# Optimization experiments

Measured on AMD Instinct MI355X. Metric: run time of the kernel, lower is better.

The kernel has to match this reference:

```python
import jax, jax.numpy as jnp
import numpy as np

B, F, T, D, W = 65536, 8, 60, 10, 6  # batch, features, time, window, n_windows
EPS = 1e-8
BN_EPS = 1e-5
IU, JU = np.triu_indices(F, k=1)  # 28 feature pairs


def _bn1d(x, g, b):
    # training-mode BatchNorm1d over [B, C, L]: stats over (B, L) per channel
    m = x.mean(axis=(0, 2), keepdims=True)
    v = x.var(axis=(0, 2), keepdims=True)
    return (x - m) * jax.lax.rsqrt(v + BN_EPS) * g[None, :, None] + b[None, :, None]


def setup_inputs() -> dict:
    key = jax.random.key(0)
    ks = jax.random.split(key, 8)
    s = 0.1
    return {
        "xb": jax.random.normal(ks[0], (B, 1, F, T), dtype=jnp.float32),
        "conv_w": jax.random.normal(ks[1], (4, 1, 1, D), dtype=jnp.float32) * s,
        "conv_b": jnp.zeros((4,), jnp.float32),
        "bn1_g": jnp.ones((28,), jnp.float32), "bn1_b": jnp.zeros((28,), jnp.float32),
        "bn4_g": jnp.ones((F,), jnp.float32), "bn4_b": jnp.zeros((F,), jnp.float32),
        "bn6_g": jnp.ones((F,), jnp.float32), "bn6_b": jnp.zeros((F,), jnp.float32),
        "bn9_g": jnp.ones((32,), jnp.float32), "bn9_b": jnp.zeros((32,), jnp.float32),
        "bnmax_g": jnp.ones((76,), jnp.float32), "bnmax_b": jnp.zeros((76,), jnp.float32),
        "w1": jax.random.normal(ks[2], (30, 608), dtype=jnp.float32) * s,
        "b1": jnp.zeros((30,), jnp.float32),
        "w2": jax.random.normal(ks[3], (1, 30), dtype=jnp.float32) * s,
        "b2": jnp.zeros((1,), jnp.float32),
    }


def reference(xb, conv_w, conv_b, bn1_g, bn1_b, bn4_g, bn4_b, bn6_g, bn6_b,
              bn9_g, bn9_b, bnmax_g, bnmax_b, w1, b1, w2, b2):
    b = xb.shape[0]
    xw = xb.reshape(b, F, W, D)  # non-overlapping windows of length D=10

    # ts_corr: pairwise Pearson correlation per window -> [b, 28, W]
    mu = xw.mean(axis=-1, keepdims=True)
    c = xw - mu
    cov = jnp.einsum('bfwt,bgwt->bfgw', c, c) / D          # [b,F,F,W]
    std = jnp.sqrt((c * c).mean(axis=-1) + EPS)            # [b,F,W]
    corr = cov / (std[:, :, None, :] * std[:, None, :, :] + EPS)
    xb1 = corr[:, IU, JU, :]                               # [b,28,W]

    # ts_zscore: mean/std per window -> [b, F, W]
    xb4 = mu[..., 0] / (std + EPS)

    # ts_decaylinear: linear-decay weighted mean -> [b, F, W]
    dw = jnp.arange(1, D + 1, dtype=jnp.float32)
    dw = dw / dw.sum()
    xb6 = jnp.einsum('bfwt,t->bfw', xw, dw)

    # conv2d kernel (1,10) stride (1,10) -> [b, 4*F, W]
    xb9 = jnp.einsum('bfwt,ot->bofw', xw, conv_w[:, 0, 0, :]) + conv_b[None, :, None, None]
    xb9 = xb9.reshape(b, 4 * F, W)

    h = jnp.concatenate([
        _bn1d(xb1, bn1_g, bn1_b),
        _bn1d(xb4, bn4_g, bn4_b),
        _bn1d(xb6, bn6_g, bn6_b),
        _bn1d(xb9, bn9_g, bn9_b),
    ], axis=1)                                             # [b,76,6]

    h_max = h.reshape(b, 76, 2, 3).max(axis=-1)            # MaxPool1d(3,3) -> [b,76,2]
    h_max = _bn1d(h_max, bnmax_g, bnmax_b)

    flat = jnp.concatenate([h.reshape(b, -1), h_max.reshape(b, -1)], axis=1)  # [b,608]
    out = jax.nn.relu(flat @ w1.T + b1) @ w2.T + b2
    return out.reshape(-1)
```

## Files before the change

kernel.cpp:

```cpp
#include <hip/hip_runtime.h>


#define EPS_F    1e-8f
#define BN_EPS_F 1e-5f
#define LSTR 82

__device__ __forceinline__ float frcp(float x) {
  return __builtin_amdgcn_rcpf(x);
}

template<int Ctrl, int RowMask>
__device__ __forceinline__ float dpp_mov0(float v) {
  return __int_as_float(__builtin_amdgcn_update_dpp(
      0, __float_as_int(v), Ctrl, RowMask, 0xf, true));
}
__device__ __forceinline__ float wave_sum64(float v) {
  v += dpp_mov0<0x111, 0xf>(v);
  v += dpp_mov0<0x112, 0xf>(v);
  v += dpp_mov0<0x114, 0xf>(v);
  v += dpp_mov0<0x118, 0xf>(v);
  v += dpp_mov0<0x142, 0xa>(v);
  v += dpp_mov0<0x143, 0xc>(v);
  return v;
}

constexpr int PI_[28] = {0,0,0,0,0,0,0, 1,1,1,1,1,1, 2,2,2,2,2, 3,3,3,3, 4,4,4, 5,5, 6};
constexpr int PJ_[28] = {1,2,3,4,5,6,7, 2,3,4,5,6,7, 3,4,5,6,7, 4,5,6,7, 5,6,7, 6,7, 7};

template<int PASS, int W>
__device__ __forceinline__ void corr_step(
    const float* __restrict__ bx, const int w,
    const float* __restrict__ w1s,
    float* __restrict__ S, float* __restrict__ Q, float* __restrict__ M,
    float* __restrict__ A, float* __restrict__ partial,
    const int bid, const int lane)
{
  constexpr int PLO = W * 14;
  constexpr int FLO = W * 4;
  float sum[8], SD[8], SP[14];
  #pragma unroll
  for (int f = 0; f < 8; ++f) { sum[f] = 0.f; SD[f] = 0.f; }
  #pragma unroll
  for (int k = 0; k < 14; ++k) SP[k] = 0.f;
  #pragma unroll
  for (int tp = 0; tp < 5; ++tp) {
    float2 x2[8];
    #pragma unroll
    for (int f = 0; f < 8; ++f)
      x2[f] = *reinterpret_cast<const float2*>(bx + f*10 + tp*2);
    #pragma unroll
    for (int f = 0; f < 8; ++f) {
      sum[f] += x2[f].x + x2[f].y;
      SD[f] = fmaf(x2[f].x, x2[f].x, fmaf(x2[f].y, x2[f].y, SD[f]));
    }
    #pragma unroll
    for (int k = 0; k < 14; ++k) {
      const int i = PI_[PLO + k], j = PJ_[PLO + k];
      SP[k] = fmaf(x2[i].x, x2[j].x, fmaf(x2[i].y, x2[j].y, SP[k]));
    }
  }
  float mu[8], sd[8];
  #pragma unroll
  for (int f = 0; f < 8; ++f) {
    mu[f] = sum[f] * 0.1f;
    sd[f] = sqrtf(fmaf(-mu[f], mu[f], SD[f] * 0.1f) + EPS_F);
  }
  #pragma unroll
  for (int k = 0; k < 14; ++k) {
    const int i = PI_[PLO + k], j = PJ_[PLO + k];
    float cov = fmaf(-mu[i], mu[j], SP[k] * 0.1f);
    float v = cov * frcp(fmaf(sd[i], sd[j], EPS_F));
    M[k] = fmaxf(M[k], v);
    if (PASS == 0) { S[k] += v; Q[k] = fmaf(v, v, Q[k]); }
    else {
      const float* wr = w1s + ((PLO + k)*6 + w) * 30;
      #pragma unroll
      for (int j2 = 0; j2 < 30; ++j2) A[j2] = fmaf(v, wr[j2], A[j2]);
    }
  }
  #pragma unroll
  for (int q = 0; q < 4; ++q) {
    const int k = 14 + q;
    float v = mu[FLO + q] * frcp(sd[FLO + q] + EPS_F);
    M[k] = fmaxf(M[k], v);
    if (PASS == 0) { S[k] += v; Q[k] = fmaf(v, v, Q[k]); }
    else {
      const float* wr = w1s + ((28 + FLO + q)*6 + w) * 30;
      #pragma unroll
      for (int j2 = 0; j2 < 30; ++j2) A[j2] = fmaf(v, wr[j2], A[j2]);
    }
  }
  if (w == 2 || w == 5) {
    const int h = (w == 5);
    #pragma unroll
    for (int k = 0; k < 18; ++k) {
      const int ch = (k < 14) ? (PLO + k) : (28 + FLO + (k - 14));
      if (PASS == 0) {
        float t2 = wave_sum64(M[k]);
        float t3 = wave_sum64(M[k] * M[k]);
        if (lane == 63) {
          partial[(size_t)(152 + ch) * 2048 + h*1024 + bid] = t2;
          partial[(size_t)(228 + ch) * 2048 + h*1024 + bid] = t3;
        }
      } else {
        const float* wr = w1s + (456 + ch*2 + h) * 30;
        #pragma unroll
        for (int j2 = 0; j2 < 30; ++j2) A[j2] = fmaf(M[k], wr[j2], A[j2]);
      }
      M[k] = -3.0e38f;
    }
  }
}

template<int PASS>
__device__ __forceinline__ void bc_step(
    const float* __restrict__ bx, const int w, const int G,
    const float* __restrict__ cw, const float* __restrict__ cb,
    const float* __restrict__ w1s,
    float* __restrict__ S, float* __restrict__ Q, float* __restrict__ M,
    float* __restrict__ A, float* __restrict__ partial,
    const int bid, const int lane)
{
  const int FLO = G * 4;
  #pragma unroll
  for (int q = 0; q < 4; ++q) {
    const int f = FLO + q;
    float2 x2[5];
    #pragma unroll
    for (int tp = 0; tp < 5; ++tp)
      x2[tp] = *reinterpret_cast<const float2*>(bx + f*10 + tp*2);
    float wsm = 0.f;
    #pragma unroll
    for (int tp = 0; tp < 5; ++tp)
      wsm = fmaf(x2[tp].x, (float)(2*tp+1) * (1.f/55.f),
            fmaf(x2[tp].y, (float)(2*tp+2) * (1.f/55.f), wsm));
    {
      const int k = q*5;
      M[k] = fmaxf(M[k], wsm);
      if (PASS == 0) { S[k] += wsm; Q[k] = fmaf(wsm, wsm, Q[k]); }
      else {
        const float* wr = w1s + ((36 + f)*6 + w) * 30;
        #pragma unroll
        for (int j2 = 0; j2 < 30; ++j2) A[j2] = fmaf(wsm, wr[j2], A[j2]);
      }
    }
    #pragma unroll
    for (int o = 0; o < 4; ++o) {
      float cv = cb[o];
      #pragma unroll
      for (int tp = 0; tp < 5; ++tp)
        cv = fmaf(x2[tp].x, cw[o*10 + 2*tp], fmaf(x2[tp].y, cw[o*10 + 2*tp + 1], cv));
      const int k = q*5 + 1 + o;
      M[k] = fmaxf(M[k], cv);
      if (PASS == 0) { S[k] += cv; Q[k] = fmaf(cv, cv, Q[k]); }
      else {
        const float* wr = w1s + ((44 + o*8 + f)*6 + w) * 30;
        #pragma unroll
        for (int j2 = 0; j2 < 30; ++j2) A[j2] = fmaf(cv, wr[j2], A[j2]);
      }
    }
  }
  if (w == 2 || w == 5) {
    const int h = (w == 5);
    #pragma unroll
    for (int k = 0; k < 20; ++k) {
      const int f = FLO + k/5, c = k%5;
      const int ch = (c == 0) ? (36 + f) : (44 + (c-1)*8 + f);
      if (PASS == 0) {
        float t2 = wave_sum64(M[k]);
        float t3 = wave_sum64(M[k] * M[k]);
        if (lane == 63) {
          partial[(size_t)(152 + ch) * 2048 + h*1024 + bid] = t2;
          partial[(size_t)(228 + ch) * 2048 + h*1024 + bid] = t3;
        }
      } else {
        const float* wr = w1s + (456 + ch*2 + h) * 30;
        #pragma unroll
        for (int j2 = 0; j2 < 30; ++j2) A[j2] = fmaf(M[k], wr[j2], A[j2]);
      }
      M[k] = -3.0e38f;
    }
  }
}


template<int PASS>
__global__ void __launch_bounds__(256, 2)
apass(const float* __restrict__ xb, const float* __restrict__ cw,
      const float* __restrict__ cb, const float* __restrict__ w1s,
      const float* __restrict__ c0, const float* __restrict__ w2,
      const float* __restrict__ b2, float* __restrict__ partial,
      float* __restrict__ out)
{
  __shared__ float sx[64 * LSTR];
  const int tid  = threadIdx.x;
  const int wave = __builtin_amdgcn_readfirstlane(tid >> 6);
  const int lane = tid & 63;
  const int bid  = blockIdx.x;

  float A[30], S[20], Q[20], M[20];
  if (PASS == 0) {
    #pragma unroll
    for (int k = 0; k < 20; ++k) { S[k] = 0.f; Q[k] = 0.f; }
  } else {
    #pragma unroll
    for (int j = 0; j < 30; ++j) A[j] = 0.f;
  }
  #pragma unroll
  for (int k = 0; k < 20; ++k) M[k] = -3.0e38f;

  const int sq = tid >> 2, qq = tid & 3;
  const float* gbase = xb + (size_t)bid * (64*480) + sq*480 + qq*120;
  float* lbase = sx + sq*LSTR + qq*20;
  const float* bx = sx + lane * LSTR;

  #pragma unroll 1
  for (int w = 0; w < 6; ++w) {
    float2 t[10];
    #pragma unroll
    for (int k = 0; k < 10; ++k)
      t[k] = *reinterpret_cast<const float2*>(gbase + w*10 + (k/5)*60 + (k%5)*2);
    #pragma unroll
    for (int k = 0; k < 10; ++k)
      *reinterpret_cast<float2*>(lbase + (k/5)*10 + (k%5)*2) = t[k];
    __syncthreads();
    if      (wave == 0) corr_step<PASS,0>(bx, w, w1s, S, Q, M, A, partial, bid, lane);
    else if (wave == 1) corr_step<PASS,1>(bx, w, w1s, S, Q, M, A, partial, bid, lane);
    else                bc_step<PASS>(bx, w, wave - 2, cw, cb, w1s, S, Q, M, A,
                                      partial, bid, lane);
    __syncthreads();
  }

  if (PASS == 0) {
    const int nch = (wave < 2) ? 18 : 20;
    #pragma unroll
    for (int k = 0; k < 20; ++k) {
      if (k < nch) {
        int ch;
        if (wave < 2) ch = (k < 14) ? (wave*14 + k) : (28 + wave*4 + (k - 14));
        else {
          const int f = (wave - 2)*4 + k/5, c = k%5;
          ch = (c == 0) ? (36 + f) : (44 + (c-1)*8 + f);
        }
        float t0 = wave_sum64(S[k]);
        float t1 = wave_sum64(Q[k]);
        if (lane == 63) {
          partial[(size_t)ch * 2048 + bid]        = t0;
          partial[(size_t)(76 + ch) * 2048 + bid] = t1;
        }
      }
    }
  } else {
    if (wave >= 2) {
      #pragma unroll
      for (int j = 0; j < 30; ++j) sx[((wave - 2)*64 + lane)*31 + j] = A[j];
    }
    __syncthreads();
    if (wave < 2) {
      #pragma unroll
      for (int j = 0; j < 30; ++j) A[j] += sx[(wave*64 + lane)*31 + j];
    }
    __syncthreads();
    if (wave == 1) {
      #pragma unroll
      for (int j = 0; j < 30; ++j) sx[lane*31 + j] = A[j];
    }
    __syncthreads();
    if (wave == 0) {
      float t = b2[0];
      #pragma unroll
      for (int j = 0; j < 30; ++j) {
        float hh = A[j] + sx[lane*31 + j] + c0[j];
        t = fmaf(w2[j], fmaxf(hh, 0.f), t);
      }
      out[bid * 64 + lane] = t;
    }
  }
}

__global__ void __launch_bounds__(256)
kR(const float* __restrict__ partial, float* __restrict__ stats) {
  const int r = blockIdx.x;
  const float* p = partial + (size_t)r * 2048;
  const int tid = threadIdx.x;
  float s = 0.f;
  #pragma unroll
  for (int i = 0; i < 8; ++i) s += p[i*256 + tid];
  s = wave_sum64(s);
  __shared__ float ls[4];
  if ((tid & 63) == 63) ls[tid >> 6] = s;
  __syncthreads();
  if (tid == 0) stats[r] = (ls[0] + ls[1]) + (ls[2] + ls[3]);
}


__global__ void k2_params(const float* __restrict__ stats,
    const float* __restrict__ bn1g, const float* __restrict__ bn1b,
    const float* __restrict__ bn4g, const float* __restrict__ bn4b,
    const float* __restrict__ bn6g, const float* __restrict__ bn6b,
    const float* __restrict__ bn9g, const float* __restrict__ bn9b,
    const float* __restrict__ bnmg, const float* __restrict__ bnmb,
    float* __restrict__ params) {
  int c = threadIdx.x;
  if (c >= 76) return;
  float g, b;
  if      (c < 28) { g = bn1g[c];    b = bn1b[c];    }
  else if (c < 36) { g = bn4g[c-28]; b = bn4b[c-28]; }
  else if (c < 44) { g = bn6g[c-36]; b = bn6b[c-36]; }
  else             { g = bn9g[c-44]; b = bn9b[c-44]; }
  const float in1 = 1.0f / (65536.0f * 6.0f);
  const float in2 = 1.0f / (65536.0f * 2.0f);
  float mean = stats[c] * in1;
  float var  = stats[76 + c] * in1 - mean * mean;
  float r    = rsqrtf(var + BN_EPS_F);
  float sc1  = g * r;
  float sh1  = b - mean * sc1;
  float mmr  = stats[152 + c] * in2;
  float vmr  = stats[228 + c] * in2 - mmr * mmr;
  float meanm = sc1 * mmr + sh1;
  float varm  = sc1 * sc1 * vmr;
  float rm  = rsqrtf(varm + BN_EPS_F);
  float scm = bnmg[c] * rm;
  float shm = bnmb[c] - meanm * scm;
  params[c]        = sc1;
  params[76 + c]   = sh1;
  params[152 + c]  = scm;
  params[228 + c]  = shm;
}

__device__ __forceinline__ void row_scale(const float* __restrict__ params,
                                          int r, float& sc, float& cst) {
  if (r < 456) {
    int c = r / 6;
    sc = params[c]; cst = params[76 + c];
  } else {
    int c = (r - 456) >> 1;
    float sc1 = params[c], sh1 = params[76 + c];
    float scm = params[152 + c], shm = params[228 + c];
    sc = sc1 * scm; cst = fmaf(scm, sh1, shm);
  }
}

__global__ void k2b(const float* __restrict__ w1, const float* __restrict__ params,
                    float* __restrict__ w1s) {
  int r = blockIdx.x;
  int j = threadIdx.x;
  float sc, cst;
  row_scale(params, r, sc, cst);
  if (j < 30) w1s[r * 30 + j] = sc * w1[j * 608 + r];
}

__global__ void k2c(const float* __restrict__ w1, const float* __restrict__ params,
                    const float* __restrict__ b1, float* __restrict__ c0) {
  const int j = blockIdx.x;
  const int lane = threadIdx.x;
  float s = 0.f;
  for (int r = lane; r < 608; r += 64) {
    float sc, cst;
    row_scale(params, r, sc, cst);
    s = fmaf(cst, w1[j * 608 + r], s);
  }
  s = wave_sum64(s);
  if (lane == 63) c0[j] = s + b1[j];
}


extern "C" void kernel_launch(void* const* d_in, const int* in_sizes, int n_in,
                              void* d_out, int out_size, void* d_ws, size_t ws_size,
                              hipStream_t stream) {
  (void)in_sizes; (void)n_in; (void)out_size; (void)ws_size;
  const float* xb   = (const float*)d_in[0];
  const float* cw   = (const float*)d_in[1];
  const float* cb   = (const float*)d_in[2];
  const float* bn1g = (const float*)d_in[3];
  const float* bn1b = (const float*)d_in[4];
  const float* bn4g = (const float*)d_in[5];
  const float* bn4b = (const float*)d_in[6];
  const float* bn6g = (const float*)d_in[7];
  const float* bn6b = (const float*)d_in[8];
  const float* bn9g = (const float*)d_in[9];
  const float* bn9b = (const float*)d_in[10];
  const float* bnmg = (const float*)d_in[11];
  const float* bnmb = (const float*)d_in[12];
  const float* w1   = (const float*)d_in[13];
  const float* b1   = (const float*)d_in[14];
  const float* w2   = (const float*)d_in[15];
  const float* b2   = (const float*)d_in[16];

  float* out     = (float*)d_out;
  float* ws      = (float*)d_ws;
  float* stats   = ws;
  float* params  = ws + 304;
  float* c0      = ws + 608;
  float* w1s     = ws + 640;
  float* partial = ws + 18880;

  hipMemsetAsync(partial, 0, (size_t)304 * 2048 * sizeof(float), stream);
  apass<0><<<1024, 256, 0, stream>>>(xb, cw, cb, nullptr, nullptr, nullptr,
                                     nullptr, partial, nullptr);
  kR<<<304, 256, 0, stream>>>(partial, stats);
  k2_params<<<1, 128, 0, stream>>>(stats, bn1g, bn1b, bn4g, bn4b, bn6g, bn6b,
                                   bn9g, bn9b, bnmg, bnmb, params);
  k2b<<<608, 32, 0, stream>>>(w1, params, w1s);
  k2c<<<30, 64, 0, stream>>>(w1, params, b1, c0);
  apass<1><<<1024, 256, 0, stream>>>(xb, cw, cb, w1s, c0, w2, b2,
                                     nullptr, out);
}
```

Before: 406.8 us.

## Prefetch next window during compute, compact partials, merge param kernels

```diff
diff --git a/kernel.cpp b/kernel.cpp
--- a/kernel.cpp
+++ b/kernel.cpp
@@ -99,8 +99,8 @@
         float t2 = wave_sum64(M[k]);
         float t3 = wave_sum64(M[k] * M[k]);
         if (lane == 63) {
-          partial[(size_t)(152 + ch) * 2048 + h*1024 + bid] = t2;
-          partial[(size_t)(228 + ch) * 2048 + h*1024 + bid] = t3;
+          partial[(size_t)(152*1024) + (size_t)ch * 2048 + h*1024 + bid] = t2;
+          partial[(size_t)(152*1024) + (size_t)(76 + ch) * 2048 + h*1024 + bid] = t3;
         }
       } else {
         const float* wr = w1s + (456 + ch*2 + h) * 30;
@@ -170,8 +170,8 @@
         float t2 = wave_sum64(M[k]);
         float t3 = wave_sum64(M[k] * M[k]);
         if (lane == 63) {
-          partial[(size_t)(152 + ch) * 2048 + h*1024 + bid] = t2;
-          partial[(size_t)(228 + ch) * 2048 + h*1024 + bid] = t3;
+          partial[(size_t)(152*1024) + (size_t)ch * 2048 + h*1024 + bid] = t2;
+          partial[(size_t)(152*1024) + (size_t)(76 + ch) * 2048 + h*1024 + bid] = t3;
         }
       } else {
         const float* wr = w1s + (456 + ch*2 + h) * 30;
@@ -214,21 +214,33 @@
   float* lbase = sx + sq*LSTR + qq*20;
   const float* bx = sx + lane * LSTR;
 
+  float2 t[10];
+  #pragma unroll
+  for (int k = 0; k < 10; ++k)
+    t[k] = *reinterpret_cast<const float2*>(gbase + (k/5)*60 + (k%5)*2);
+  #pragma unroll
+  for (int k = 0; k < 10; ++k)
+    *reinterpret_cast<float2*>(lbase + (k/5)*10 + (k%5)*2) = t[k];
+  __syncthreads();
+
   #pragma unroll 1
   for (int w = 0; w < 6; ++w) {
-    float2 t[10];
-    #pragma unroll
-    for (int k = 0; k < 10; ++k)
-      t[k] = *reinterpret_cast<const float2*>(gbase + w*10 + (k/5)*60 + (k%5)*2);
-    #pragma unroll
-    for (int k = 0; k < 10; ++k)
-      *reinterpret_cast<float2*>(lbase + (k/5)*10 + (k%5)*2) = t[k];
-    __syncthreads();
+    if (w < 5) {
+      #pragma unroll
+      for (int k = 0; k < 10; ++k)
+        t[k] = *reinterpret_cast<const float2*>(gbase + (w+1)*10 + (k/5)*60 + (k%5)*2);
+    }
     if      (wave == 0) corr_step<PASS,0>(bx, w, w1s, S, Q, M, A, partial, bid, lane);
     else if (wave == 1) corr_step<PASS,1>(bx, w, w1s, S, Q, M, A, partial, bid, lane);
     else                bc_step<PASS>(bx, w, wave - 2, cw, cb, w1s, S, Q, M, A,
                                       partial, bid, lane);
     __syncthreads();
+    if (w < 5) {
+      #pragma unroll
+      for (int k = 0; k < 10; ++k)
+        *reinterpret_cast<float2*>(lbase + (k/5)*10 + (k%5)*2) = t[k];
+      __syncthreads();
+    }
   }
 
   if (PASS == 0) {
@@ -245,8 +257,8 @@
         float t0 = wave_sum64(S[k]);
         float t1 = wave_sum64(Q[k]);
         if (lane == 63) {
-          partial[(size_t)ch * 2048 + bid]        = t0;
-          partial[(size_t)(76 + ch) * 2048 + bid] = t1;
+          partial[(size_t)ch * 1024 + bid]        = t0;
+          partial[(size_t)(76 + ch) * 1024 + bid] = t1;
         }
       }
     }
@@ -267,13 +279,13 @@
     }
     __syncthreads();
     if (wave == 0) {
-      float t = b2[0];
+      float t0 = b2[0];
       #pragma unroll
       for (int j = 0; j < 30; ++j) {
         float hh = A[j] + sx[lane*31 + j] + c0[j];
-        t = fmaf(w2[j], fmaxf(hh, 0.f), t);
-      }
-      out[bid * 64 + lane] = t;
+        t0 = fmaf(w2[j], fmaxf(hh, 0.f), t0);
+      }
+      out[bid * 64 + lane] = t0;
     }
   }
 }
@@ -281,11 +293,17 @@
 __global__ void __launch_bounds__(256)
 kR(const float* __restrict__ partial, float* __restrict__ stats) {
   const int r = blockIdx.x;
-  const float* p = partial + (size_t)r * 2048;
   const int tid = threadIdx.x;
   float s = 0.f;
-  #pragma unroll
-  for (int i = 0; i < 8; ++i) s += p[i*256 + tid];
+  if (r < 152) {
+    const float* p = partial + (size_t)r * 1024;
+    #pragma unroll
+    for (int i = 0; i < 4; ++i) s += p[i*256 + tid];
+  } else {
+    const float* p = partial + (size_t)(152*1024) + (size_t)(r - 152) * 2048;
+    #pragma unroll
+    for (int i = 0; i < 8; ++i) s += p[i*256 + tid];
+  }
   s = wave_sum64(s);
   __shared__ float ls[4];
   if ((tid & 63) == 63) ls[tid >> 6] = s;
@@ -293,75 +311,70 @@
   if (tid == 0) stats[r] = (ls[0] + ls[1]) + (ls[2] + ls[3]);
 }
 
-
-__global__ void k2_params(const float* __restrict__ stats,
-    const float* __restrict__ bn1g, const float* __restrict__ bn1b,
-    const float* __restrict__ bn4g, const float* __restrict__ bn4b,
-    const float* __restrict__ bn6g, const float* __restrict__ bn6b,
-    const float* __restrict__ bn9g, const float* __restrict__ bn9b,
-    const float* __restrict__ bnmg, const float* __restrict__ bnmb,
-    float* __restrict__ params) {
-  int c = threadIdx.x;
-  if (c >= 76) return;
-  float g, b;
-  if      (c < 28) { g = bn1g[c];    b = bn1b[c];    }
-  else if (c < 36) { g = bn4g[c-28]; b = bn4b[c-28]; }
-  else if (c < 44) { g = bn6g[c-36]; b = bn6b[c-36]; }
-  else             { g = bn9g[c-44]; b = bn9b[c-44]; }
-  const float in1 = 1.0f / (65536.0f * 6.0f);
-  const float in2 = 1.0f / (65536.0f * 2.0f);
-  float mean = stats[c] * in1;
-  float var  = stats[76 + c] * in1 - mean * mean;
-  float r    = rsqrtf(var + BN_EPS_F);
-  float sc1  = g * r;
-  float sh1  = b - mean * sc1;
-  float mmr  = stats[152 + c] * in2;
-  float vmr  = stats[228 + c] * in2 - mmr * mmr;
-  float meanm = sc1 * mmr + sh1;
-  float varm  = sc1 * sc1 * vmr;
-  float rm  = rsqrtf(varm + BN_EPS_F);
-  float scm = bnmg[c] * rm;
-  float shm = bnmb[c] - meanm * scm;
-  params[c]        = sc1;
-  params[76 + c]   = sh1;
-  params[152 + c]  = scm;
-  params[228 + c]  = shm;
-}
-
-__device__ __forceinline__ void row_scale(const float* __restrict__ params,
-                                          int r, float& sc, float& cst) {
-  if (r < 456) {
-    int c = r / 6;
-    sc = params[c]; cst = params[76 + c];
+__global__ void __launch_bounds__(256)
+k2(const float* __restrict__ stats,
+   const float* __restrict__ bn1g, const float* __restrict__ bn1b,
+   const float* __restrict__ bn4g, const float* __restrict__ bn4b,
+   const float* __restrict__ bn6g, const float* __restrict__ bn6b,
+   const float* __restrict__ bn9g, const float* __restrict__ bn9b,
+   const float* __restrict__ bnmg, const float* __restrict__ bnmb,
+   const float* __restrict__ w1, const float* __restrict__ b1,
+   float* __restrict__ w1s, float* __restrict__ c0) {
+  __shared__ float P0[76], P1[76], P2[76], P3[76];
+  const int tid = threadIdx.x;
+  if (tid < 76) {
+    const int c = tid;
+    float g, b;
+    if      (c < 28) { g = bn1g[c];    b = bn1b[c];    }
+    else if (c < 36) { g = bn4g[c-28]; b = bn4b[c-28]; }
+    else if (c < 44) { g = bn6g[c-36]; b = bn6b[c-36]; }
+    else             { g = bn9g[c-44]; b = bn9b[c-44]; }
+    const float in1 = 1.0f / (65536.0f * 6.0f);
+    const float in2 = 1.0f / (65536.0f * 2.0f);
+    float mean = stats[c] * in1;
+    float var  = stats[76 + c] * in1 - mean * mean;
+    float r    = rsqrtf(var + BN_EPS_F);
+    float sc1  = g * r;
+    float sh1  = b - mean * sc1;
+    float mmr  = stats[152 + c] * in2;
+    float vmr  = stats[228 + c] * in2 - mmr * mmr;
+    float meanm = sc1 * mmr + sh1;
+    float varm  = sc1 * sc1 * vmr;
+    float rm  = rsqrtf(varm + BN_EPS_F);
+    float scm = bnmg[c] * rm;
+    float shm = bnmb[c] - meanm * scm;
+    P0[c] = sc1; P1[c] = sh1; P2[c] = scm; P3[c] = shm;
+  }
+  __syncthreads();
+
+  if (blockIdx.x < 38) {
+    const int r0 = blockIdx.x * 16;
+    for (int e = tid; e < 16*30; e += 256) {
+      const int r = r0 + e / 30, j = e % 30;
+      float sc;
+      if (r < 456) sc = P0[r / 6];
+      else { const int c = (r - 456) >> 1; sc = P0[c] * P2[c]; }
+      w1s[r * 30 + j] = sc * w1[j * 608 + r];
+    }
   } else {
-    int c = (r - 456) >> 1;
-    float sc1 = params[c], sh1 = params[76 + c];
-    float scm = params[152 + c], shm = params[228 + c];
-    sc = sc1 * scm; cst = fmaf(scm, sh1, shm);
-  }
-}
-
-__global__ void k2b(const float* __restrict__ w1, const float* __restrict__ params,
-                    float* __restrict__ w1s) {
-  int r = blockIdx.x;
-  int j = threadIdx.x;
-  float sc, cst;
-  row_scale(params, r, sc, cst);
-  if (j < 30) w1s[r * 30 + j] = sc * w1[j * 608 + r];
-}
-
-__global__ void k2c(const float* __restrict__ w1, const float* __restrict__ params,
-                    const float* __restrict__ b1, float* __restrict__ c0) {
-  const int j = blockIdx.x;
-  const int lane = threadIdx.x;
-  float s = 0.f;
-  for (int r = lane; r < 608; r += 64) {
-    float sc, cst;
-    row_scale(params, r, sc, cst);
-    s = fmaf(cst, w1[j * 608 + r], s);
-  }
-  s = wave_sum64(s);
-  if (lane == 63) c0[j] = s + b1[j];
+    const int j = tid >> 3, l8 = tid & 7;
+    if (j < 30) {
+      float s = 0.f;
+      for (int r = l8; r < 608; r += 8) {
+        float cst;
+        if (r < 456) cst = P1[r / 6];
+        else {
+          const int c = (r - 456) >> 1;
+          cst = fmaf(P2[c], P1[c], P3[c]);
+        }
+        s = fmaf(cst, w1[j * 608 + r], s);
+      }
+      s += __shfl_xor(s, 1, 64);
+      s += __shfl_xor(s, 2, 64);
+      s += __shfl_xor(s, 4, 64);
+      if (l8 == 0) c0[j] = s + b1[j];
+    }
+  }
 }
 
 
@@ -390,19 +403,15 @@
   float* out     = (float*)d_out;
   float* ws      = (float*)d_ws;
   float* stats   = ws;
-  float* params  = ws + 304;
   float* c0      = ws + 608;
   float* w1s     = ws + 640;
   float* partial = ws + 18880;
 
-  hipMemsetAsync(partial, 0, (size_t)304 * 2048 * sizeof(float), stream);
   apass<0><<<1024, 256, 0, stream>>>(xb, cw, cb, nullptr, nullptr, nullptr,
                                      nullptr, partial, nullptr);
   kR<<<304, 256, 0, stream>>>(partial, stats);
-  k2_params<<<1, 128, 0, stream>>>(stats, bn1g, bn1b, bn4g, bn4b, bn6g, bn6b,
-                                   bn9g, bn9b, bnmg, bnmb, params);
-  k2b<<<608, 32, 0, stream>>>(w1, params, w1s);
-  k2c<<<30, 64, 0, stream>>>(w1, params, b1, c0);
+  k2<<<39, 256, 0, stream>>>(stats, bn1g, bn1b, bn4g, bn4b, bn6g, bn6b,
+                             bn9g, bn9b, bnmg, bnmb, w1, b1, w1s, c0);
   apass<1><<<1024, 256, 0, stream>>>(xb, cw, cb, w1s, c0, w2, b2,
                                      nullptr, out);
 }
```

After: 398.9 us. About the same (-2.0%).
